# Kernel tuning notes

Hardware: AMD Instinct MI355X
Metric: run time of the kernel (lower is better)

The kernel has to match this reference:

```python
import jax, jax.numpy as jnp
import numpy as np

B, T, D = 4, 2048, 1024
F = 4 * D  # Config.RWKV_INTERMIDATE_SIZE * hidden_dim
LN_EPS = 1e-3  # keras LayerNormalization default epsilon


def layer_norm(x, g, b, eps=LN_EPS):
    mu = jnp.mean(x, axis=-1, keepdims=True)
    var = jnp.mean(jnp.square(x - mu), axis=-1, keepdims=True)
    return (x - mu) * jax.lax.rsqrt(var + eps) * g + b


def setup_inputs() -> dict:
    ks = jax.random.split(jax.random.key(0), 24)
    g = lambda k, shape: (jax.random.normal(k, shape, jnp.float32)
                          * np.sqrt(2.0 / sum(shape)))  # ~glorot
    return {
        "x": jax.random.normal(ks[0], (B, T, D), jnp.float32),
        "s_cm": jnp.zeros((B, D), jnp.float32),
        "s_tm": jnp.zeros((B, D), jnp.float32),
        "s_num": jnp.zeros((B, D), jnp.float32),
        "s_den": jnp.zeros((B, D), jnp.float32),
        "s_q": jnp.zeros((B, D), jnp.float32),
        "ln1_g": jnp.ones((D,), jnp.float32),
        "ln1_b": jnp.zeros((D,), jnp.float32),
        "ln2_g": jnp.ones((D,), jnp.float32),
        "ln2_b": jnp.zeros((D,), jnp.float32),
        "tm_mix_k": jax.random.uniform(ks[1], (D,), jnp.float32, 0.0, 2.0 / D),
        "tm_mix_v": jax.random.uniform(ks[2], (D,), jnp.float32, 0.0, 2.0 / D),
        "tm_mix_r": jax.random.uniform(ks[3], (D,), jnp.float32, 0.0, (2.0 / D) ** 0.5),
        "tm_kw": g(ks[4], (D, D)),
        "tm_vw": g(ks[5], (D, D)),
        "tm_rw": g(ks[6], (D, D)),
        "time_decay": jax.random.uniform(ks[7], (D,), jnp.float32, 0.0, 0.1),
        "time_first": jax.random.uniform(ks[8], (D,), jnp.float32, 0.0, 0.05),
        "out_w": g(ks[9], (D, D)),
        "cm_mix_k": jax.random.uniform(ks[10], (D,), jnp.float32, 0.0, 2.0 / D),
        "cm_mix_r": jax.random.uniform(ks[11], (D,), jnp.float32, 0.0, 2.0 / D),
        "cm_kw": g(ks[12], (D, F)),
        "cm_vw": g(ks[13], (F, D)),
        "cm_rw": g(ks[14], (D, D)),
    }


def _shift(h, s):
    # token shift: prepend last-token state, drop last timestep
    return jnp.concatenate([s[:, None, :], h[:, :-1, :]], axis=1)


def reference(x, s_cm, s_tm, s_num, s_den, s_q,
              ln1_g, ln1_b, ln2_g, ln2_b,
              tm_mix_k, tm_mix_v, tm_mix_r, tm_kw, tm_vw, tm_rw,
              time_decay, time_first, out_w,
              cm_mix_k, cm_mix_r, cm_kw, cm_vw, cm_rw):
    # ---- time mixing ----
    h = layer_norm(x, ln1_g, ln1_b)  # [B,T,D]
    hs = _shift(h, s_tm)
    xk = h * tm_mix_k + hs * (1.0 - tm_mix_k)
    xv = h * tm_mix_v + hs * (1.0 - tm_mix_v)
    xr = h * tm_mix_r + hs * (1.0 - tm_mix_r)
    k = xk @ tm_kw  # [B,T,D]
    v = xv @ tm_vw
    r = jax.nn.sigmoid(xr @ tm_rw)
    w = -jnp.exp(time_decay)  # [D]

    def step(carry, kv):
        num, den, q = carry
        kt, vt = kv  # [B,D]
        mo = jnp.maximum(q, kt + time_first)
        e1 = jnp.exp(q - mo)
        e2 = jnp.exp(kt + time_first - mo)
        out = (e1 * num + e2 * vt) / (e1 * den + e2)
        ms = jnp.maximum(q + w, kt)
        e1s = jnp.exp(q + w - ms)
        e2s = jnp.exp(kt - ms)
        return (e1s * num + e2s * vt, e1s * den + e2s, ms), out

    (num, den, q), wkv = jax.lax.scan(
        step, (s_num, s_den, s_q),
        (k.transpose(1, 0, 2), v.transpose(1, 0, 2)))
    wkv = wkv.transpose(1, 0, 2)  # [B,T,D]
    x = x + (r * wkv) @ out_w

    # ---- channel mixing ----
    h2 = layer_norm(x, ln2_g, ln2_b)
    hs2 = _shift(h2, s_cm)
    xk2 = h2 * cm_mix_k + hs2 * (1.0 - cm_mix_k)
    xr2 = h2 * cm_mix_r + hs2 * (1.0 - cm_mix_r)
    kv = jnp.square(jax.nn.relu(xk2 @ cm_kw)) @ cm_vw  # [B,T,F] -> [B,T,D]
    x = x + jax.nn.sigmoid(xr2 @ cm_rw) * kv

    # new state: (cm_inputs, tm_inputs, num, den, q)
    return x, h2[:, -1], h[:, -1], num, den, q
```

## Files before the change

### kernel.cpp

```cpp
#include <hip/hip_runtime.h>

typedef unsigned short ushort_t;
typedef __attribute__((ext_vector_type(8))) short short8;
typedef __attribute__((ext_vector_type(4))) float f32x4;

#define B_ 4
#define T_ 2048
#define D_ 1024
#define F_ 4096
#define M_ (B_*T_)
#define CH_ 64
#define NC_ (T_/CH_)

#define AS1 __attribute__((address_space(1)))
#define AS3 __attribute__((address_space(3)))

__device__ __forceinline__ ushort_t f2bf(float f) {
  union { float f; unsigned u; } a; a.f = f;
  unsigned r = a.u + 0x7FFFu + ((a.u >> 16) & 1u);
  return (ushort_t)(r >> 16);
}

__device__ __forceinline__ float bf2f(ushort_t u) {
  union { unsigned u; float f; } a; a.u = ((unsigned)u) << 16;
  return a.f;
}

__device__ __forceinline__ void gl_lds16(const void* g, void* l) {
  __builtin_amdgcn_global_load_lds((AS1 void*)(__UINTPTR_TYPE__)g,
                                   (AS3 void*)l, 16, 0, 0);
}

__device__ __forceinline__ void xcd_swz(int gx, int gy, int& bx, int& by, int& bz) {
  int lid = blockIdx.x + gx * (blockIdx.y + gy * blockIdx.z);
  int nwg = gx * gy * gridDim.z;
  int cpx = nwg >> 3;
  int L = (lid & 7) * cpx + (lid >> 3);
  int gy4 = (gy >= 4) ? (gy >> 2) : 1;
  by = (L & 3) + 4 * ((L >> 4) % gy4);
  int bxz = ((L >> 2) & 3) + 4 * (L / (4 * gy));
  bx = bxz % gx;
  bz = bxz / gx;
}

__global__ __launch_bounds__(256) void tconv(const float* __restrict__ W,
                                             ushort_t* __restrict__ Wt,
                                             int K, int N) {
  __shared__ float tile[32][33];
  int tx = threadIdx.x, ty = threadIdx.y;
  int n0 = blockIdx.x * 32, k0 = blockIdx.y * 32;
  #pragma unroll
  for (int i = 0; i < 32; i += 8)
    tile[ty + i][tx] = W[(size_t)(k0 + ty + i) * N + n0 + tx];
  __syncthreads();
  #pragma unroll
  for (int i = 0; i < 32; i += 8)
    Wt[(size_t)(n0 + ty + i) * K + k0 + tx] = f2bf(tile[tx][ty + i]);
}

__global__ __launch_bounds__(256) void tconv5(const float* __restrict__ s0,
                                              const float* __restrict__ s1,
                                              const float* __restrict__ s2,
                                              const float* __restrict__ s3,
                                              const float* __restrict__ s4,
                                              ushort_t* __restrict__ d0,
                                              ushort_t* __restrict__ d1,
                                              ushort_t* __restrict__ d2,
                                              ushort_t* __restrict__ d3,
                                              ushort_t* __restrict__ d4) {
  __shared__ float tile[32][33];
  int z = blockIdx.z;
  const float* W = (z == 0) ? s0 : (z == 1) ? s1 : (z == 2) ? s2 : (z == 3) ? s3 : s4;
  ushort_t* Wt   = (z == 0) ? d0 : (z == 1) ? d1 : (z == 2) ? d2 : (z == 3) ? d3 : d4;
  int tx = threadIdx.x, ty = threadIdx.y;
  int n0 = blockIdx.x * 32, k0 = blockIdx.y * 32;
  #pragma unroll
  for (int i = 0; i < 32; i += 8)
    tile[ty + i][tx] = W[(size_t)(k0 + ty + i) * D_ + n0 + tx];
  __syncthreads();
  #pragma unroll
  for (int i = 0; i < 32; i += 8)
    Wt[(size_t)(n0 + ty + i) * D_ + k0 + tx] = f2bf(tile[tx][ty + i]);
}

#define MIX1(c, p, f) f2bf((c) * (f) + (p) * (1.0f - (f)))

template <int NOUT>
__global__ __launch_bounds__(256)
void ln_mix(const float* __restrict__ xin, const float* __restrict__ st,
            const float* __restrict__ g, const float* __restrict__ bb,
            const float* __restrict__ mk, const float* __restrict__ mv,
            const float* __restrict__ mr,
            ushort_t* __restrict__ ok, ushort_t* __restrict__ ov,
            ushort_t* __restrict__ orr, float* __restrict__ last) {
  int row = blockIdx.x;
  int t = row & (T_ - 1);
  int b = row >> 11;
  int tid = threadIdx.x;
  const bool pln = (t != 0);
  float4 vc = ((const float4*)(xin + (size_t)row * D_))[tid];
  float4 vp = pln ? ((const float4*)(xin + (size_t)(row - 1) * D_))[tid]
                  : ((const float4*)(st + (size_t)b * D_))[tid];
  float s0 = vc.x + vc.y + vc.z + vc.w;
  float s1 = vc.x * vc.x + vc.y * vc.y + vc.z * vc.z + vc.w * vc.w;
  float s2 = vp.x + vp.y + vp.z + vp.w;
  float s3 = vp.x * vp.x + vp.y * vp.y + vp.z * vp.z + vp.w * vp.w;
  #pragma unroll
  for (int o = 32; o > 0; o >>= 1) {
    s0 += __shfl_down(s0, o); s1 += __shfl_down(s1, o);
    s2 += __shfl_down(s2, o); s3 += __shfl_down(s3, o);
  }
  __shared__ float red[4][4];
  if ((tid & 63) == 0) {
    int w = tid >> 6;
    red[w][0] = s0; red[w][1] = s1; red[w][2] = s2; red[w][3] = s3;
  }
  __syncthreads();
  float cs0 = red[0][0] + red[1][0] + red[2][0] + red[3][0];
  float cs1 = red[0][1] + red[1][1] + red[2][1] + red[3][1];
  float ps0 = red[0][2] + red[1][2] + red[2][2] + red[3][2];
  float ps1 = red[0][3] + red[1][3] + red[2][3] + red[3][3];

  float mu = cs0 * (1.0f / D_);
  float rs = rsqrtf(cs1 * (1.0f / D_) - mu * mu + 1e-3f);
  float4 gv = ((const float4*)g)[tid];
  float4 bv = ((const float4*)bb)[tid];
  float hc[4], hp[4];
  hc[0] = (vc.x - mu) * rs * gv.x + bv.x;
  hc[1] = (vc.y - mu) * rs * gv.y + bv.y;
  hc[2] = (vc.z - mu) * rs * gv.z + bv.z;
  hc[3] = (vc.w - mu) * rs * gv.w + bv.w;
  if (pln) {
    float mup = ps0 * (1.0f / D_);
    float rsp = rsqrtf(ps1 * (1.0f / D_) - mup * mup + 1e-3f);
    hp[0] = (vp.x - mup) * rsp * gv.x + bv.x;
    hp[1] = (vp.y - mup) * rsp * gv.y + bv.y;
    hp[2] = (vp.z - mup) * rsp * gv.z + bv.z;
    hp[3] = (vp.w - mup) * rsp * gv.w + bv.w;
  } else {
    hp[0] = vp.x; hp[1] = vp.y; hp[2] = vp.z; hp[3] = vp.w;
  }

  size_t qi = (size_t)row * 256 + tid;
  float4 k4 = ((const float4*)mk)[tid];
  float4 r4 = ((const float4*)mr)[tid];
  ushort4 o4;
  o4.x = MIX1(hc[0], hp[0], k4.x); o4.y = MIX1(hc[1], hp[1], k4.y);
  o4.z = MIX1(hc[2], hp[2], k4.z); o4.w = MIX1(hc[3], hp[3], k4.w);
  ((ushort4*)ok)[qi] = o4;
  if (NOUT == 3) {
    float4 v4 = ((const float4*)mv)[tid];
    o4.x = MIX1(hc[0], hp[0], v4.x); o4.y = MIX1(hc[1], hp[1], v4.y);
    o4.z = MIX1(hc[2], hp[2], v4.z); o4.w = MIX1(hc[3], hp[3], v4.w);
    ((ushort4*)ov)[qi] = o4;
  }
  o4.x = MIX1(hc[0], hp[0], r4.x); o4.y = MIX1(hc[1], hp[1], r4.y);
  o4.z = MIX1(hc[2], hp[2], r4.z); o4.w = MIX1(hc[3], hp[3], r4.w);
  ((ushort4*)orr)[qi] = o4;

  if (t == T_ - 1) {
    float4 h4; h4.x = hc[0]; h4.y = hc[1]; h4.z = hc[2]; h4.w = hc[3];
    ((float4*)(last + (size_t)b * D_))[tid] = h4;
  }
}

__global__ __launch_bounds__(256) void wkv_part1(const ushort_t* __restrict__ k,
                                                 const ushort_t* __restrict__ v,
                                                 const float* __restrict__ tdec,
                                                 float* __restrict__ cn,
                                                 float* __restrict__ cd,
                                                 float* __restrict__ cq) {
  int idx = blockIdx.x * 256 + threadIdx.x;
  int d = idx & (D_ - 1);
  int b = (idx >> 10) & (B_ - 1);
  int c = idx >> 12;
  float w = -__expf(tdec[d]);
  const ushort_t* kp = k + ((size_t)b * T_ + c * CH_) * D_ + d;
  const ushort_t* vp = v + ((size_t)b * T_ + c * CH_) * D_ + d;
  float num = 0.0f, den = 0.0f, q = -1e30f;
  for (int t0 = 0; t0 < CH_; t0 += 8) {
    float kt[8], vt[8];
    #pragma unroll
    for (int i = 0; i < 8; ++i) {
      size_t off = (size_t)(t0 + i) * D_;
      kt[i] = bf2f(kp[off]); vt[i] = bf2f(vp[off]);
    }
    #pragma unroll
    for (int i = 0; i < 8; ++i) {
      float kk = kt[i];
      float ms = fmaxf(q + w, kk);
      float e1 = __expf(q + w - ms), e2 = __expf(kk - ms);
      num = e1 * num + e2 * vt[i];
      den = e1 * den + e2;
      q = ms;
    }
  }
  cn[idx] = num; cd[idx] = den; cq[idx] = q;
}

__global__ __launch_bounds__(256) void wkv_part2(const float* __restrict__ cn,
                                                 const float* __restrict__ cd,
                                                 const float* __restrict__ cq,
                                                 const float* __restrict__ sn,
                                                 const float* __restrict__ sd,
                                                 const float* __restrict__ sq,
                                                 const float* __restrict__ tdec,
                                                 float* __restrict__ pn,
                                                 float* __restrict__ pd,
                                                 float* __restrict__ pq,
                                                 float* __restrict__ on,
                                                 float* __restrict__ od,
                                                 float* __restrict__ oq) {
  int idx = blockIdx.x * 256 + threadIdx.x;
  int d = idx & (D_ - 1);
  float w = -__expf(tdec[d]);
  float wL = w * (float)CH_;
  float num = sn[idx], den = sd[idx], q = sq[idx];
  #pragma unroll 4
  for (int c = 0; c < NC_; ++c) {
    int j = (c << 12) + idx;
    pn[j] = num; pd[j] = den; pq[j] = q;
    float m2 = cq[j];
    float qn = fmaxf(q + wL, m2);
    float e1 = __expf(q + wL - qn), e2 = __expf(m2 - qn);
    num = e1 * num + e2 * cn[j];
    den = e1 * den + e2 * cd[j];
    q = qn;
  }
  on[idx] = num; od[idx] = den; oq[idx] = q;
}

__global__ __launch_bounds__(256) void wkv_part3(const ushort_t* __restrict__ k,
                                                 const ushort_t* __restrict__ v,
                                                 const float* __restrict__ ra,
                                                 const float* __restrict__ rb,
                                                 const float* __restrict__ pn,
                                                 const float* __restrict__ pd,
                                                 const float* __restrict__ pq,
                                                 const float* __restrict__ tdec,
                                                 const float* __restrict__ tfirst,
                                                 ushort_t* __restrict__ rwkv) {
  int idx = blockIdx.x * 256 + threadIdx.x;
  int d = idx & (D_ - 1);
  int b = (idx >> 10) & (B_ - 1);
  int c = idx >> 12;
  float w = -__expf(tdec[d]);
  float tf = tfirst[d];
  float num = pn[idx], den = pd[idx], q = pq[idx];
  size_t base = ((size_t)b * T_ + c * CH_) * D_ + d;
  const ushort_t* kp = k + base;
  const ushort_t* vp = v + base;
  const float* rap = ra + base;
  const float* rbp = rb + base;
  ushort_t* op = rwkv + base;
  for (int t0 = 0; t0 < CH_; t0 += 8) {
    float kt[8], vt[8], rt[8];
    #pragma unroll
    for (int i = 0; i < 8; ++i) {
      size_t off = (size_t)(t0 + i) * D_;
      kt[i] = bf2f(kp[off]); vt[i] = bf2f(vp[off]);
      rt[i] = 1.0f / (1.0f + __expf(-(rap[off] + rbp[off])));
    }
    #pragma unroll
    for (int i = 0; i < 8; ++i) {
      float kk = kt[i];
      float mo = fmaxf(q, kk + tf);
      float e1 = __expf(q - mo), e2 = __expf(kk + tf - mo);
      float o = (e1 * num + e2 * vt[i]) / (e1 * den + e2);
      op[(size_t)(t0 + i) * D_] = f2bf(rt[i] * o);
      float ms = fmaxf(q + w, kk);
      float e1s = __expf(q + w - ms), e2s = __expf(kk - ms);
      num = e1s * num + e2s * vt[i];
      den = e1s * den + e2s;
      q = ms;
    }
  }
}

template <int EPI>
__global__ __launch_bounds__(512, 2)
void gemm256(const ushort_t* __restrict__ A, const ushort_t* __restrict__ Bt,
             int N, int K, int ktn,
             float* __restrict__ Cf, float* __restrict__ Cf2,
             ushort_t* __restrict__ Ub) {
  __shared__ alignas(16) ushort_t sA[2][256 * 64];
  __shared__ alignas(16) ushort_t sB[2][256 * 64];
  const int tid = threadIdx.x;
  const int lane = tid & 63;
  const int wave = tid >> 6;
  const int wr = wave >> 2, wc = wave & 3;
  const int l15 = lane & 15;
  const int kb = (lane >> 4) << 4;
  int bx, by, bz;
  xcd_swz(gridDim.x, gridDim.y, bx, by, bz);
  const int m0 = bx * 256, n0 = by * 256;
  const int kt0 = (EPI == 0) ? bz * ktn : 0;

  const ushort_t* Ause = A;
  const ushort_t* Buse = Bt;
  if (EPI == 3) {
    Ause = A + (size_t)bz * M_ * D_;
    Buse = Bt + (size_t)bz * D_ * D_;
  }
  const ushort_t* gA = Ause + (size_t)m0 * K + (size_t)kt0 * 64;
  const ushort_t* gB = Buse + (size_t)n0 * K + (size_t)kt0 * 64;

  const int sr = tid >> 3;
  const int sc8 = (tid & 7) ^ (sr & 7);
  const int scb = (tid & 7) * 16;

  auto stage = [&](int dbuf, int kt, int h) {
    const ushort_t* g = (h < 2) ? gA : gB;
    ushort_t* sb = (h < 2) ? sA[dbuf] : sB[dbuf];
    int rbase = (h & 1) * 128;
    #pragma unroll
    for (int i = 0; i < 2; ++i) {
      int row = rbase + i * 64 + sr;
      gl_lds16(g + (size_t)row * K + (size_t)kt * 64 + sc8 * 8,
               (char*)sb + row * 128 + scb);
    }
  };

  auto ld = [&](const ushort_t* sbuf, int row, int s5) -> short8 {
    int cb = ((s5 << 6) + kb) ^ ((row & 7) << 4);
    return *(const short8*)((const char*)sbuf + row * 128 + cb);
  };

  f32x4 acc[8][4] = {};

  stage(0, 0, 0); stage(0, 0, 1); stage(0, 0, 2); stage(0, 0, 3);

  for (int t = 0; t < ktn; ++t) {
    const int cur = t & 1, nxt = cur ^ 1;
    const bool more = (t + 1 < ktn);
    if (more) { stage(nxt, t + 1, 0); stage(nxt, t + 1, 1); }
    if (more) asm volatile("s_waitcnt vmcnt(4)" ::: "memory");
    else      asm volatile("s_waitcnt vmcnt(0)" ::: "memory");
    __builtin_amdgcn_s_barrier();

    const ushort_t* curA = sA[cur];
    const ushort_t* curB = sB[cur];
    short8 bfr[4][2];

#define G256_MFMA16(MI0, A00, A01, A10, A11)                                  \
    __builtin_amdgcn_s_setprio(1);                                            \
    _Pragma("unroll")                                                         \
    for (int ni = 0; ni < 4; ++ni) {                                          \
      acc[MI0][ni] = __builtin_amdgcn_mfma_f32_16x16x32_bf16(                 \
          A00, bfr[ni][0], acc[MI0][ni], 0, 0, 0);                            \
      acc[MI0][ni] = __builtin_amdgcn_mfma_f32_16x16x32_bf16(                 \
          A01, bfr[ni][1], acc[MI0][ni], 0, 0, 0);                            \
      acc[MI0 + 1][ni] = __builtin_amdgcn_mfma_f32_16x16x32_bf16(             \
          A10, bfr[ni][0], acc[MI0 + 1][ni], 0, 0, 0);                        \
      acc[MI0 + 1][ni] = __builtin_amdgcn_mfma_f32_16x16x32_bf16(             \
          A11, bfr[ni][1], acc[MI0 + 1][ni], 0, 0, 0);                        \
    }                                                                         \
    __builtin_amdgcn_s_setprio(0);

#define G256_SYNC_IN()                                                        \
    asm volatile("" ::: "memory");                                            \
    __builtin_amdgcn_s_barrier();                                             \
    asm volatile("s_waitcnt lgkmcnt(0)" ::: "memory");                        \
    __builtin_amdgcn_sched_barrier(0);

#define G256_SYNC_OUT()                                                       \
    asm volatile("" ::: "memory");                                            \
    __builtin_amdgcn_s_barrier();

    {
      #pragma unroll
      for (int ni = 0; ni < 4; ++ni)
        #pragma unroll
        for (int s = 0; s < 2; ++s)
          bfr[ni][s] = ld(curB, wc * 64 + ni * 16 + l15, s);
      short8 a00 = ld(curA, wr * 128 + 0 * 16 + l15, 0);
      short8 a01 = ld(curA, wr * 128 + 0 * 16 + l15, 1);
      short8 a10 = ld(curA, wr * 128 + 1 * 16 + l15, 0);
      short8 a11 = ld(curA, wr * 128 + 1 * 16 + l15, 1);
      if (more) stage(nxt, t + 1, 2);
      G256_SYNC_IN();
      G256_MFMA16(0, a00, a01, a10, a11);
      G256_SYNC_OUT();
    }
    {
      short8 a00 = ld(curA, wr * 128 + 2 * 16 + l15, 0);
      short8 a01 = ld(curA, wr * 128 + 2 * 16 + l15, 1);
      short8 a10 = ld(curA, wr * 128 + 3 * 16 + l15, 0);
      short8 a11 = ld(curA, wr * 128 + 3 * 16 + l15, 1);
      if (more) stage(nxt, t + 1, 3);
      G256_SYNC_IN();
      G256_MFMA16(2, a00, a01, a10, a11);
      G256_SYNC_OUT();
    }
    {
      short8 a00 = ld(curA, wr * 128 + 4 * 16 + l15, 0);
      short8 a01 = ld(curA, wr * 128 + 4 * 16 + l15, 1);
      short8 a10 = ld(curA, wr * 128 + 5 * 16 + l15, 0);
      short8 a11 = ld(curA, wr * 128 + 5 * 16 + l15, 1);
      G256_SYNC_IN();
      G256_MFMA16(4, a00, a01, a10, a11);
      G256_SYNC_OUT();
    }
    {
      short8 a00 = ld(curA, wr * 128 + 6 * 16 + l15, 0);
      short8 a01 = ld(curA, wr * 128 + 6 * 16 + l15, 1);
      short8 a10 = ld(curA, wr * 128 + 7 * 16 + l15, 0);
      short8 a11 = ld(curA, wr * 128 + 7 * 16 + l15, 1);
      G256_SYNC_IN();
      G256_MFMA16(6, a00, a01, a10, a11);
      G256_SYNC_OUT();
    }
  }

  float* cfp = (EPI == 0 && bz) ? Cf2 : Cf;
  ushort_t* ub = Ub;
  if (EPI == 3) ub = Ub + (size_t)bz * M_ * D_;
  #pragma unroll
  for (int mi = 0; mi < 8; ++mi)
    #pragma unroll
    for (int ni = 0; ni < 4; ++ni)
      #pragma unroll
      for (int j = 0; j < 4; ++j) {
        int row = m0 + wr * 128 + mi * 16 + ((lane >> 4) << 2) + j;
        int col = n0 + wc * 64 + ni * 16 + l15;
        size_t idx = (size_t)row * N + col;
        float v = acc[mi][ni][j];
        if (EPI == 0) {
          cfp[idx] = v;
        } else if (EPI == 1) {
          float tt = v > 0.0f ? v : 0.0f;
          ub[idx] = f2bf(tt * tt);
        } else if (EPI == 3) {
          ub[idx] = f2bf(v);
        }
      }
}

template <int EPI>
__global__ __launch_bounds__(512, 2)
void gemmB(const ushort_t* __restrict__ A, const ushort_t* __restrict__ Bt,
           int K, int ktn,
           float* __restrict__ Cf,
           const float* __restrict__ X, const float* __restrict__ X2,
           const float* __restrict__ Xb) {
  __shared__ alignas(16) ushort_t sA[2][128 * 64];
  __shared__ alignas(16) ushort_t sB[2][256 * 64];
  const int tid = threadIdx.x;
  const int lane = tid & 63;
  const int wave = tid >> 6;
  const int wr = wave >> 2, wc = wave & 3;
  const int l15 = lane & 15;
  const int kb = (lane >> 4) << 4;
  int bx, by, zid;
  xcd_swz(gridDim.x, gridDim.y, bx, by, zid);
  const int m0 = bx * 128, n0 = by * 256;

  const ushort_t* gA = A + (size_t)m0 * K;
  const ushort_t* gB = Bt + (size_t)n0 * K;

  const int sr = tid >> 3;
  const int sc8 = (tid & 7) ^ (sr & 7);
  const int scb = (tid & 7) * 16;

  auto stage = [&](int dbuf, int kt, int h) {
    if (h < 2) {
      int row = h * 64 + sr;
      gl_lds16(gA + (size_t)row * K + (size_t)kt * 64 + sc8 * 8,
               (char*)sA[dbuf] + row * 128 + scb);
    } else {
      int rbase = (h - 2) * 128;
      #pragma unroll
      for (int i = 0; i < 2; ++i) {
        int row = rbase + i * 64 + sr;
        gl_lds16(gB + (size_t)row * K + (size_t)kt * 64 + sc8 * 8,
                 (char*)sB[dbuf] + row * 128 + scb);
      }
    }
  };

  auto ld = [&](const ushort_t* sbuf, int row, int s5) -> short8 {
    int cb = ((s5 << 6) + kb) ^ ((row & 7) << 4);
    return *(const short8*)((const char*)sbuf + row * 128 + cb);
  };

  f32x4 acc[4][4] = {};

  stage(0, 0, 0); stage(0, 0, 1); stage(0, 0, 2); stage(0, 0, 3);

  for (int t = 0; t < ktn; ++t) {
    const int cur = t & 1, nxt = cur ^ 1;
    const bool more = (t + 1 < ktn);
    if (more) {
      stage(nxt, t + 1, 0); stage(nxt, t + 1, 1);
      stage(nxt, t + 1, 2); stage(nxt, t + 1, 3);
    }
    if (more) asm volatile("s_waitcnt vmcnt(6)" ::: "memory");
    else      asm volatile("s_waitcnt vmcnt(0)" ::: "memory");
    __builtin_amdgcn_s_barrier();

    const ushort_t* curA = sA[cur];
    const ushort_t* curB = sB[cur];

    #pragma unroll
    for (int s = 0; s < 2; ++s) {
      short8 av[4], bv[4];
      #pragma unroll
      for (int i = 0; i < 4; ++i) av[i] = ld(curA, wr * 64 + i * 16 + l15, s);
      #pragma unroll
      for (int i = 0; i < 4; ++i) bv[i] = ld(curB, wc * 64 + i * 16 + l15, s);
      asm volatile("" ::: "memory");
      __builtin_amdgcn_s_barrier();
      asm volatile("s_waitcnt lgkmcnt(0)" ::: "memory");
      __builtin_amdgcn_sched_barrier(0);
      __builtin_amdgcn_s_setprio(1);
      #pragma unroll
      for (int mi = 0; mi < 4; ++mi)
        #pragma unroll
        for (int ni = 0; ni < 4; ++ni)
          acc[mi][ni] = __builtin_amdgcn_mfma_f32_16x16x32_bf16(
              av[mi], bv[ni], acc[mi][ni], 0, 0, 0);
      __builtin_amdgcn_s_setprio(0);
      asm volatile("" ::: "memory");
      __builtin_amdgcn_s_barrier();
    }
  }

  #pragma unroll
  for (int mi = 0; mi < 4; ++mi)
    #pragma unroll
    for (int ni = 0; ni < 4; ++ni)
      #pragma unroll
      for (int j = 0; j < 4; ++j) {
        int row = m0 + wr * 64 + mi * 16 + ((lane >> 4) << 2) + j;
        int col = n0 + wc * 64 + ni * 16 + l15;
        size_t idx = (size_t)row * D_ + col;
        float v = acc[mi][ni][j];
        if (EPI == 2) {
          Cf[idx] = X[idx] + v;
        } else if (EPI == 4) {
          float s = 1.0f / (1.0f + __expf(-v));
          Cf[idx] = X2[idx] + s * (X[idx] + Xb[idx]);
        }
      }
}

extern "C" void kernel_launch(void* const* d_in, const int* in_sizes, int n_in,
                              void* d_out, int out_size, void* d_ws, size_t ws_size,
                              hipStream_t stream) {
  const float* x      = (const float*)d_in[0];
  const float* s_cm   = (const float*)d_in[1];
  const float* s_tm   = (const float*)d_in[2];
  const float* s_num  = (const float*)d_in[3];
  const float* s_den  = (const float*)d_in[4];
  const float* s_q    = (const float*)d_in[5];
  const float* ln1_g  = (const float*)d_in[6];
  const float* ln1_b  = (const float*)d_in[7];
  const float* ln2_g  = (const float*)d_in[8];
  const float* ln2_b  = (const float*)d_in[9];
  const float* tmk    = (const float*)d_in[10];
  const float* tmv    = (const float*)d_in[11];
  const float* tmr    = (const float*)d_in[12];
  const float* tm_kw  = (const float*)d_in[13];
  const float* tm_vw  = (const float*)d_in[14];
  const float* tm_rw  = (const float*)d_in[15];
  const float* tdec   = (const float*)d_in[16];
  const float* tfirst = (const float*)d_in[17];
  const float* out_w  = (const float*)d_in[18];
  const float* cmk    = (const float*)d_in[19];
  const float* cmr    = (const float*)d_in[20];
  const float* cm_kw  = (const float*)d_in[21];
  const float* cm_vw  = (const float*)d_in[22];
  const float* cm_rw  = (const float*)d_in[23];

  float* out   = (float*)d_out;
  float* o_x   = out;
  float* o_h2l = out + (size_t)M_ * D_;
  float* o_hl  = o_h2l + B_ * D_;
  float* o_num = o_hl + B_ * D_;
  float* o_den = o_num + B_ * D_;
  float* o_q   = o_den + B_ * D_;

  char* W = (char*)d_ws;
  const size_t MB = 1024 * 1024;
  ushort_t* w_tmk = (ushort_t*)(W + 0 * MB);
  ushort_t* w_tmv = (ushort_t*)(W + 2 * MB);
  ushort_t* w_tmr = (ushort_t*)(W + 4 * MB);
  ushort_t* w_out = (ushort_t*)(W + 6 * MB);
  ushort_t* w_cmk = (ushort_t*)(W + 8 * MB);
  ushort_t* w_cmv = (ushort_t*)(W + 16 * MB);
  ushort_t* w_cmr = (ushort_t*)(W + 24 * MB);
  float* cn = (float*)(W + 26 * MB + 0 * 512 * 1024);
  float* cd = (float*)(W + 26 * MB + 1 * 512 * 1024);
  float* cq = (float*)(W + 26 * MB + 2 * 512 * 1024);
  float* pn = (float*)(W + 26 * MB + 3 * 512 * 1024);
  float* pd = (float*)(W + 26 * MB + 4 * 512 * 1024);
  float* pq = (float*)(W + 26 * MB + 5 * 512 * 1024);
  ushort_t* xk    = (ushort_t*)(W + 32 * MB);
  ushort_t* xv    = (ushort_t*)(W + 48 * MB);
  ushort_t* xr    = (ushort_t*)(W + 64 * MB);
  ushort_t* kbuf  = (ushort_t*)(W + 80 * MB);
  ushort_t* vbuf  = (ushort_t*)(W + 96 * MB);
  ushort_t* kk    = (ushort_t*)(W + 128 * MB);
  float*    ra    = (float*)(W + 32 * MB);
  float*    rb    = (float*)(W + 128 * MB);
  float*    kv_a  = (float*)(W + 64 * MB);
  float*    kv_b  = (float*)(W + 96 * MB);
  ushort_t* rwkv  = xr;
  ushort_t* xk2   = xk;
  ushort_t* xr2   = xv;

  dim3 tb(32, 8);
  tconv5<<<dim3(D_/32, D_/32, 5), tb, 0, stream>>>(tm_kw, tm_vw, tm_rw, out_w, cm_rw,
                                                   w_tmk, w_tmv, w_tmr, w_out, w_cmr);
  tconv<<<dim3(F_/32, D_/32), tb, 0, stream>>>(cm_kw, w_cmk, D_, F_);
  tconv<<<dim3(D_/32, F_/32), tb, 0, stream>>>(cm_vw, w_cmv, F_, D_);

  ln_mix<3><<<M_, 256, 0, stream>>>(x, s_tm, ln1_g, ln1_b, tmk, tmv, tmr,
                                    xk, xv, xr, o_hl);
  gemm256<3><<<dim3(M_/256, D_/256, 2), 512, 0, stream>>>(
      xk, w_tmk, D_, D_, D_/64, nullptr, nullptr, kbuf);
  gemm256<0><<<dim3(M_/256, D_/256, 2), 512, 0, stream>>>(
      xr, w_tmr, D_, D_, D_/128, ra, rb, nullptr);

  wkv_part1<<<(NC_ * B_ * D_) / 256, 256, 0, stream>>>(kbuf, vbuf, tdec, cn, cd, cq);
  wkv_part2<<<(B_ * D_) / 256, 256, 0, stream>>>(cn, cd, cq, s_num, s_den, s_q, tdec,
                                                 pn, pd, pq, o_num, o_den, o_q);
  wkv_part3<<<(NC_ * B_ * D_) / 256, 256, 0, stream>>>(kbuf, vbuf, ra, rb, pn, pd, pq,
                                                       tdec, tfirst, rwkv);

  gemmB<2><<<dim3(M_/128, D_/256, 1), 512, 0, stream>>>(
      rwkv, w_out, D_, D_/64, o_x, x, nullptr, nullptr);

  ln_mix<2><<<M_, 256, 0, stream>>>(o_x, s_cm, ln2_g, ln2_b, cmk, nullptr, cmr,
                                    xk2, nullptr, xr2, o_h2l);
  gemm256<1><<<dim3(M_/256, F_/256, 1), 512, 0, stream>>>(
      xk2, w_cmk, F_, D_, D_/64, nullptr, nullptr, kk);
  gemm256<0><<<dim3(M_/256, D_/256, 2), 512, 0, stream>>>(
      kk, w_cmv, D_, F_, F_/128, kv_a, kv_b, nullptr);
  gemmB<4><<<dim3(M_/128, D_/256, 1), 512, 0, stream>>>(
      xr2, w_cmr, D_, D_/64, o_x, kv_a, o_x, kv_b);
}
```

Baseline: 394.3 us.

## Merge k/v/r projection GEMMs into one launch with a half-depth K tile

Adds a gemm256h kernel that uses a 32-wide K tile, which halves shared memory per block. One launch with z=4 now computes the k and v projections (bf16 outputs) and the split-K r projection (two fp32 partials), replacing two separate launches. The channel-mix key GEMM with relu-square epilogue also moves to this kernel. The r partial buffers are relocated so they no longer alias xr, since the r GEMM now runs in the same launch that reads xr. The aim is to cut launch count and tail effects and to raise occupancy through smaller LDS, at the cost of more barriers per unit of K work.

```diff
diff --git a/kernel.cpp b/kernel.cpp
--- a/kernel.cpp
+++ b/kernel.cpp
@@ -279,6 +279,153 @@
 
 template <int EPI>
 __global__ __launch_bounds__(512, 2)
+void gemm256h(const ushort_t* __restrict__ A, const ushort_t* __restrict__ Bt,
+              const ushort_t* __restrict__ A2, const ushort_t* __restrict__ Bt2,
+              int N, int K,
+              float* __restrict__ Cra, float* __restrict__ Crb,
+              ushort_t* __restrict__ Ub) {
+  __shared__ alignas(16) ushort_t sA[2][256 * 32];
+  __shared__ alignas(16) ushort_t sB[2][256 * 32];
+  const int tid = threadIdx.x;
+  const int lane = tid & 63;
+  const int wave = tid >> 6;
+  const int wr = wave >> 2, wc = wave & 3;
+  const int l15 = lane & 15;
+  const int kb = (lane >> 4) << 4;
+  int bx, by, bz;
+  xcd_swz(gridDim.x, gridDim.y, bx, by, bz);
+  const int m0 = bx * 256, n0 = by * 256;
+
+  const ushort_t* gA;
+  const ushort_t* gB;
+  int ktn;
+  if (EPI == 0) {
+    if (bz < 2) {
+      gA = A + (size_t)bz * M_ * D_ + (size_t)m0 * K;
+      gB = Bt + (size_t)bz * D_ * D_ + (size_t)n0 * K;
+      ktn = K >> 5;
+    } else {
+      gA = A2 + (size_t)m0 * K + (size_t)(bz - 2) * (K >> 1);
+      gB = Bt2 + (size_t)n0 * K + (size_t)(bz - 2) * (K >> 1);
+      ktn = K >> 6;
+    }
+  } else {
+    gA = A + (size_t)m0 * K;
+    gB = Bt + (size_t)n0 * K;
+    ktn = K >> 5;
+  }
+
+  const int sr2 = tid >> 2;
+  const int sc4 = (tid & 3) ^ (sr2 & 3);
+  const int scb = (tid & 3) * 16;
+
+  auto stage = [&](int dbuf, int kt, int h) {
+    const ushort_t* g = (h < 2) ? gA : gB;
+    ushort_t* sb = (h < 2) ? sA[dbuf] : sB[dbuf];
+    int row = (h & 1) * 128 + sr2;
+    gl_lds16(g + (size_t)row * K + (size_t)kt * 32 + sc4 * 8,
+             (char*)sb + row * 64 + scb);
+  };
+
+  auto ld = [&](const ushort_t* sbuf, int row) -> short8 {
+    int cb = kb ^ ((row & 3) << 4);
+    return *(const short8*)((const char*)sbuf + row * 64 + cb);
+  };
+
+  f32x4 acc[8][4] = {};
+
+  stage(0, 0, 0); stage(0, 0, 1); stage(0, 0, 2); stage(0, 0, 3);
+
+  for (int t = 0; t < ktn; ++t) {
+    const int cur = t & 1, nxt = cur ^ 1;
+    const bool more = (t + 1 < ktn);
+    if (more) {
+      stage(nxt, t + 1, 0); stage(nxt, t + 1, 1);
+      asm volatile("s_waitcnt vmcnt(2)" ::: "memory");
+    } else {
+      asm volatile("s_waitcnt vmcnt(0)" ::: "memory");
+    }
+    __builtin_amdgcn_s_barrier();
+
+    const ushort_t* curA = sA[cur];
+    const ushort_t* curB = sB[cur];
+    short8 bfr[4];
+
+    {
+      #pragma unroll
+      for (int ni = 0; ni < 4; ++ni) bfr[ni] = ld(curB, wc * 64 + ni * 16 + l15);
+      short8 a0 = ld(curA, wr * 128 + 0 * 16 + l15);
+      short8 a1 = ld(curA, wr * 128 + 1 * 16 + l15);
+      short8 a2 = ld(curA, wr * 128 + 2 * 16 + l15);
+      short8 a3 = ld(curA, wr * 128 + 3 * 16 + l15);
+      if (more) { stage(nxt, t + 1, 2); stage(nxt, t + 1, 3); }
+      asm volatile("" ::: "memory");
+      __builtin_amdgcn_s_barrier();
+      asm volatile("s_waitcnt lgkmcnt(0)" ::: "memory");
+      __builtin_amdgcn_sched_barrier(0);
+      __builtin_amdgcn_s_setprio(1);
+      #pragma unroll
+      for (int ni = 0; ni < 4; ++ni) {
+        acc[0][ni] = __builtin_amdgcn_mfma_f32_16x16x32_bf16(a0, bfr[ni], acc[0][ni], 0, 0, 0);
+        acc[1][ni] = __builtin_amdgcn_mfma_f32_16x16x32_bf16(a1, bfr[ni], acc[1][ni], 0, 0, 0);
+        acc[2][ni] = __builtin_amdgcn_mfma_f32_16x16x32_bf16(a2, bfr[ni], acc[2][ni], 0, 0, 0);
+        acc[3][ni] = __builtin_amdgcn_mfma_f32_16x16x32_bf16(a3, bfr[ni], acc[3][ni], 0, 0, 0);
+      }
+      __builtin_amdgcn_s_setprio(0);
+      asm volatile("" ::: "memory");
+      __builtin_amdgcn_s_barrier();
+    }
+    {
+      short8 a0 = ld(curA, wr * 128 + 4 * 16 + l15);
+      short8 a1 = ld(curA, wr * 128 + 5 * 16 + l15);
+      short8 a2 = ld(curA, wr * 128 + 6 * 16 + l15);
+      short8 a3 = ld(curA, wr * 128 + 7 * 16 + l15);
+      asm volatile("" ::: "memory");
+      __builtin_amdgcn_s_barrier();
+      asm volatile("s_waitcnt lgkmcnt(0)" ::: "memory");
+      __builtin_amdgcn_sched_barrier(0);
+      __builtin_amdgcn_s_setprio(1);
+      #pragma unroll
+      for (int ni = 0; ni < 4; ++ni) {
+        acc[4][ni] = __builtin_amdgcn_mfma_f32_16x16x32_bf16(a0, bfr[ni], acc[4][ni], 0, 0, 0);
+        acc[5][ni] = __builtin_amdgcn_mfma_f32_16x16x32_bf16(a1, bfr[ni], acc[5][ni], 0, 0, 0);
+        acc[6][ni] = __builtin_amdgcn_mfma_f32_16x16x32_bf16(a2, bfr[ni], acc[6][ni], 0, 0, 0);
+        acc[7][ni] = __builtin_amdgcn_mfma_f32_16x16x32_bf16(a3, bfr[ni], acc[7][ni], 0, 0, 0);
+      }
+      __builtin_amdgcn_s_setprio(0);
+      asm volatile("" ::: "memory");
+      __builtin_amdgcn_s_barrier();
+    }
+  }
+
+  ushort_t* ub = Ub;
+  float* cfp = nullptr;
+  if (EPI == 0) {
+    if (bz < 2) ub = Ub + (size_t)bz * M_ * D_;
+    else        cfp = (bz == 2) ? Cra : Crb;
+  }
+  #pragma unroll
+  for (int mi = 0; mi < 8; ++mi)
+    #pragma unroll
+    for (int ni = 0; ni < 4; ++ni)
+      #pragma unroll
+      for (int j = 0; j < 4; ++j) {
+        int row = m0 + wr * 128 + mi * 16 + ((lane >> 4) << 2) + j;
+        int col = n0 + wc * 64 + ni * 16 + l15;
+        size_t idx = (size_t)row * N + col;
+        float v = acc[mi][ni][j];
+        if (EPI == 0) {
+          if (bz < 2) ub[idx] = f2bf(v);
+          else        cfp[idx] = v;
+        } else {
+          float tt = v > 0.0f ? v : 0.0f;
+          ub[idx] = f2bf(tt * tt);
+        }
+      }
+}
+
+template <int EPI>
+__global__ __launch_bounds__(512, 2)
 void gemm256(const ushort_t* __restrict__ A, const ushort_t* __restrict__ Bt,
              int N, int K, int ktn,
              float* __restrict__ Cf, float* __restrict__ Cf2,
@@ -294,16 +441,10 @@
   int bx, by, bz;
   xcd_swz(gridDim.x, gridDim.y, bx, by, bz);
   const int m0 = bx * 256, n0 = by * 256;
-  const int kt0 = (EPI == 0) ? bz * ktn : 0;
-
-  const ushort_t* Ause = A;
-  const ushort_t* Buse = Bt;
-  if (EPI == 3) {
-    Ause = A + (size_t)bz * M_ * D_;
-    Buse = Bt + (size_t)bz * D_ * D_;
-  }
-  const ushort_t* gA = Ause + (size_t)m0 * K + (size_t)kt0 * 64;
-  const ushort_t* gB = Buse + (size_t)n0 * K + (size_t)kt0 * 64;
+  const int kt0 = bz * ktn;
+
+  const ushort_t* gA = A + (size_t)m0 * K + (size_t)kt0 * 64;
+  const ushort_t* gB = Bt + (size_t)n0 * K + (size_t)kt0 * 64;
 
   const int sr = tid >> 3;
   const int sc8 = (tid & 7) ^ (sr & 7);
@@ -412,9 +553,7 @@
     }
   }
 
-  float* cfp = (EPI == 0 && bz) ? Cf2 : Cf;
-  ushort_t* ub = Ub;
-  if (EPI == 3) ub = Ub + (size_t)bz * M_ * D_;
+  float* cfp = bz ? Cf2 : Cf;
   #pragma unroll
   for (int mi = 0; mi < 8; ++mi)
     #pragma unroll
@@ -424,15 +563,7 @@
         int row = m0 + wr * 128 + mi * 16 + ((lane >> 4) << 2) + j;
         int col = n0 + wc * 64 + ni * 16 + l15;
         size_t idx = (size_t)row * N + col;
-        float v = acc[mi][ni][j];
-        if (EPI == 0) {
-          cfp[idx] = v;
-        } else if (EPI == 1) {
-          float tt = v > 0.0f ? v : 0.0f;
-          ub[idx] = f2bf(tt * tt);
-        } else if (EPI == 3) {
-          ub[idx] = f2bf(v);
-        }
+        cfp[idx] = acc[mi][ni][j];
       }
 }
 
@@ -601,8 +732,8 @@
   ushort_t* kbuf  = (ushort_t*)(W + 80 * MB);
   ushort_t* vbuf  = (ushort_t*)(W + 96 * MB);
   ushort_t* kk    = (ushort_t*)(W + 128 * MB);
-  float*    ra    = (float*)(W + 32 * MB);
-  float*    rb    = (float*)(W + 128 * MB);
+  float*    ra    = (float*)(W + 128 * MB);
+  float*    rb    = (float*)(W + 160 * MB);
   float*    kv_a  = (float*)(W + 64 * MB);
   float*    kv_b  = (float*)(W + 96 * MB);
   ushort_t* rwkv  = xr;
@@ -617,10 +748,8 @@
 
   ln_mix<3><<<M_, 256, 0, stream>>>(x, s_tm, ln1_g, ln1_b, tmk, tmv, tmr,
                                     xk, xv, xr, o_hl);
-  gemm256<3><<<dim3(M_/256, D_/256, 2), 512, 0, stream>>>(
-      xk, w_tmk, D_, D_, D_/64, nullptr, nullptr, kbuf);
-  gemm256<0><<<dim3(M_/256, D_/256, 2), 512, 0, stream>>>(
-      xr, w_tmr, D_, D_, D_/128, ra, rb, nullptr);
+  gemm256h<0><<<dim3(M_/256, D_/256, 4), 512, 0, stream>>>(
+      xk, w_tmk, xr, w_tmr, D_, D_, ra, rb, kbuf);
 
   wkv_part1<<<(NC_ * B_ * D_) / 256, 256, 0, stream>>>(kbuf, vbuf, tdec, cn, cd, cq);
   wkv_part2<<<(B_ * D_) / 256, 256, 0, stream>>>(cn, cd, cq, s_num, s_den, s_q, tdec,
@@ -633,8 +762,8 @@
 
   ln_mix<2><<<M_, 256, 0, stream>>>(o_x, s_cm, ln2_g, ln2_b, cmk, nullptr, cmr,
                                     xk2, nullptr, xr2, o_h2l);
-  gemm256<1><<<dim3(M_/256, F_/256, 1), 512, 0, stream>>>(
-      xk2, w_cmk, F_, D_, D_/64, nullptr, nullptr, kk);
+  gemm256h<1><<<dim3(M_/256, F_/256, 1), 512, 0, stream>>>(
+      xk2, w_cmk, nullptr, nullptr, F_, D_, nullptr, nullptr, kk);
   gemm256<0><<<dim3(M_/256, D_/256, 2), 512, 0, stream>>>(
       kk, w_cmv, D_, F_, F_/128, kv_a, kv_b, nullptr);
   gemmB<4><<<dim3(M_/128, D_/256, 1), 512, 0, stream>>>(
```

New measurement: 427.6 us. 8.5% more time.
